# Kernel tuning notes

Hardware: AMD Instinct MI355X
Metric: run time of the kernel (lower is better)

Reference implementation:

```python
import math
import jax, jax.numpy as jnp
import numpy as np

B, N, M, C, H, POS = 2, 2048, 64, 256, 8, 6
D = C // H  # head_dim = 32
SCALE = 1.0 / math.sqrt(D)
LAMDA = 1.0


def setup_inputs() -> dict:
    key = jax.random.key(0)
    ks = jax.random.split(key, 15)
    s = 0.05
    return {
        "pairwise_g": jax.random.normal(ks[0], (B, N, N, POS), jnp.float32),
        "coset_functions": jax.random.normal(ks[1], (B, N, C), jnp.float32),
        "mask": jnp.ones((B, N), dtype=bool),
        "Wq": jax.random.normal(ks[2], (C, C), jnp.float32) * s,
        "bq": jax.random.normal(ks[3], (C,), jnp.float32) * s,
        "Wk": jax.random.normal(ks[4], (C, C), jnp.float32) * s,
        "bk": jax.random.normal(ks[5], (C,), jnp.float32) * s,
        "Wl": jax.random.normal(ks[6], (C, POS), jnp.float32) * s,
        "bl": jax.random.normal(ks[7], (C,), jnp.float32) * s,
        "u": jax.random.normal(ks[8], (H, D), jnp.float32) * s,
        "v": jax.random.normal(ks[9], (H, D), jnp.float32) * s,
        "Wi": jax.random.normal(ks[10], (C, C), jnp.float32) * s,
        "bi": jax.random.normal(ks[11], (C,), jnp.float32) * s,
        "Wo": jax.random.normal(ks[12], (C, C), jnp.float32) * s,
        "bo": jax.random.normal(ks[13], (C,), jnp.float32) * s,
    }


def reference(pairwise_g, coset_functions, mask, Wq, bq, Wk, bk, Wl, bl, u, v, Wi, bi, Wo, bo):
    # ---- extract_neighbourhoods (mc_samples=M, fill=1.0 -> k == k_ball, permutation irrelevant)
    dists = jnp.linalg.norm(pairwise_g, axis=-1)                      # (B,N,N)
    dists = jnp.where(mask[:, None, :], dists, jnp.float32(1e8))
    _, nbhd_idx = jax.lax.top_k(-dists, M)                            # (B,N,M) nearest neighbors
    nbhd_pg = jnp.take_along_axis(pairwise_g, nbhd_idx[..., None], axis=2)  # (B,N,M,POS)
    gather_rows = jax.vmap(lambda arr, ix: arr[ix])                   # gather along point axis per batch
    nbhd_cf = gather_rows(coset_functions, nbhd_idx)                  # (B,N,M,C)
    nbhd_mask = gather_rows(mask, nbhd_idx)                           # (B,N,M)

    # ---- RelativePositionKernel
    Q = (coset_functions @ Wq.T + bq).reshape(B, N, H, D).transpose(0, 2, 1, 3)  # (B,H,N,D)
    K = (coset_functions @ Wk.T + bk).reshape(B, N, H, D).transpose(0, 2, 1, 3)  # (B,H,N,D)
    e = (nbhd_pg @ Wl.T + bl).reshape(B, N, M, H, D)                  # (B,N,M,H,D)

    S = jnp.einsum('bhnd,bhkd->bhnk', Q, K)                           # dense scores (as original)
    Sg = jnp.take_along_axis(S, nbhd_idx[:, None, :, :], axis=3)      # (B,H,N,M)
    e_term = jnp.einsum('bnmhd,bhnd->bhnm', e, Q + v[None, :, None, :])
    uK = jnp.einsum('hd,bhkd->bhk', u, K)                             # (B,H,N)
    uKg = jnp.take_along_axis(uK[:, :, None, :], nbhd_idx[:, None, :, :], axis=3)  # (B,H,N,M)
    A = (Sg + LAMDA * e_term + uKg) * SCALE
    A = A.transpose(0, 2, 3, 1)                                       # (B,N,M,H)

    # ---- masked softmax over neighbors
    A = jnp.where(nbhd_mask[..., None], A, jnp.float32(-1e38))
    attn = jax.nn.softmax(A, axis=2)                                  # (B,N,M,H)

    # ---- value projection + weighted sum + output linear
    Vv = (nbhd_cf @ Wi.T + bi).reshape(B, N, M, H, D)                 # (B,N,M,H,D)
    out = jnp.einsum('bnmh,bnmhd->bnhd', attn, Vv).reshape(B, N, C)
    out = out @ Wo.T + bo                                             # (B,N,c_out)
    return out
```

## Files before the change

### kernel.cpp

```cpp
#include <hip/hip_runtime.h>
#include <stdint.h>

#define NB 2
#define NN 2048
#define MM 64
#define CC 256
#define HH 8
#define DD 32
#define PP 6
#define ATT_SCALE 0.17677669529663687f

typedef __attribute__((ext_vector_type(8))) short short8;
typedef __attribute__((ext_vector_type(4))) float f32x4;

__device__ __forceinline__ uint16_t f2bf(float f) {
  union { float f; uint32_t u; } c; c.f = f;
  return (uint16_t)((c.u + 0x7fffu + ((c.u >> 16) & 1u)) >> 16);
}
__device__ __forceinline__ float blo(uint32_t u) {
  union { uint32_t u; float f; } c; c.u = u << 16; return c.f;
}
__device__ __forceinline__ float bhi(uint32_t u) {
  union { uint32_t u; float f; } c; c.u = u & 0xffff0000u; return c.f;
}
__device__ __forceinline__ short8 pack8(float4 a, float4 b) {
  short8 r;
  r[0] = (short)f2bf(a.x); r[1] = (short)f2bf(a.y);
  r[2] = (short)f2bf(a.z); r[3] = (short)f2bf(a.w);
  r[4] = (short)f2bf(b.x); r[5] = (short)f2bf(b.y);
  r[6] = (short)f2bf(b.z); r[7] = (short)f2bf(b.w);
  return r;
}

__global__ __launch_bounds__(64) void k_gemm_qkv(
    const float* __restrict__ A,
    const float* __restrict__ W0, const float* __restrict__ W1, const float* __restrict__ W2,
    const float* __restrict__ b0, const float* __restrict__ b1, const float* __restrict__ b2,
    float* __restrict__ Qo, uint16_t* __restrict__ Ko, uint16_t* __restrict__ Vo) {
  const int z = blockIdx.z;
  const float* W = (z == 0) ? W0 : ((z == 1) ? W1 : W2);
  const float* bias = (z == 0) ? b0 : ((z == 1) ? b1 : b2);

  const int lane = threadIdx.x;
  const int m = lane & 15;
  const int quad = lane >> 4;
  const int row0 = blockIdx.x * 16;
  const int c0 = blockIdx.y * 64;

  f32x4 acc0 = {0.f, 0.f, 0.f, 0.f};
  f32x4 acc1 = {0.f, 0.f, 0.f, 0.f};
  f32x4 acc2 = {0.f, 0.f, 0.f, 0.f};
  f32x4 acc3 = {0.f, 0.f, 0.f, 0.f};

#pragma unroll
  for (int k0 = 0; k0 < CC; k0 += 32) {
    const float4* ap = (const float4*)(A + (size_t)(row0 + m) * CC + k0 + quad * 8);
    const float4* bp0 = (const float4*)(W + (size_t)(c0 + 0 + m) * CC + k0 + quad * 8);
    const float4* bp1 = (const float4*)(W + (size_t)(c0 + 16 + m) * CC + k0 + quad * 8);
    const float4* bp2 = (const float4*)(W + (size_t)(c0 + 32 + m) * CC + k0 + quad * 8);
    const float4* bp3 = (const float4*)(W + (size_t)(c0 + 48 + m) * CC + k0 + quad * 8);
    const short8 a = pack8(ap[0], ap[1]);
    const short8 f0 = pack8(bp0[0], bp0[1]);
    const short8 f1 = pack8(bp1[0], bp1[1]);
    const short8 f2 = pack8(bp2[0], bp2[1]);
    const short8 f3 = pack8(bp3[0], bp3[1]);
    acc0 = __builtin_amdgcn_mfma_f32_16x16x32_bf16(a, f0, acc0, 0, 0, 0);
    acc1 = __builtin_amdgcn_mfma_f32_16x16x32_bf16(a, f1, acc1, 0, 0, 0);
    acc2 = __builtin_amdgcn_mfma_f32_16x16x32_bf16(a, f2, acc2, 0, 0, 0);
    acc3 = __builtin_amdgcn_mfma_f32_16x16x32_bf16(a, f3, acc3, 0, 0, 0);
  }

  const int orow = row0 + quad * 4;
  f32x4 accs[4] = {acc0, acc1, acc2, acc3};
#pragma unroll
  for (int f = 0; f < 4; ++f) {
    const int col = c0 + f * 16 + m;
    const float bv = bias[col];
#pragma unroll
    for (int r = 0; r < 4; ++r) {
      const float val = accs[f][r] + bv;
      const size_t o = (size_t)(orow + r) * CC + col;
      if (z == 0) Qo[o] = val;
      else if (z == 1) Ko[o] = f2bf(val);
      else Vo[o] = f2bf(val);
    }
  }
}

__global__ __launch_bounds__(64) void k_gemm_out(const uint16_t* __restrict__ A,
                                                 const float* __restrict__ W,
                                                 const float* __restrict__ bias,
                                                 float* __restrict__ O) {
  const int lane = threadIdx.x;
  const int m = lane & 15;
  const int quad = lane >> 4;
  const int row0 = blockIdx.x * 16;
  const int c0 = blockIdx.y * 32;

  f32x4 acc0 = {0.f, 0.f, 0.f, 0.f};
  f32x4 acc1 = {0.f, 0.f, 0.f, 0.f};

#pragma unroll
  for (int k0 = 0; k0 < CC; k0 += 32) {
    const short8 a = *(const short8*)(A + (size_t)(row0 + m) * CC + k0 + quad * 8);
    const float4* bp0 = (const float4*)(W + (size_t)(c0 + 0 + m) * CC + k0 + quad * 8);
    const float4* bp1 = (const float4*)(W + (size_t)(c0 + 16 + m) * CC + k0 + quad * 8);
    const short8 f0 = pack8(bp0[0], bp0[1]);
    const short8 f1 = pack8(bp1[0], bp1[1]);
    acc0 = __builtin_amdgcn_mfma_f32_16x16x32_bf16(a, f0, acc0, 0, 0, 0);
    acc1 = __builtin_amdgcn_mfma_f32_16x16x32_bf16(a, f1, acc1, 0, 0, 0);
  }

  const int orow = row0 + quad * 4;
  f32x4 accs[2] = {acc0, acc1};
#pragma unroll
  for (int f = 0; f < 2; ++f) {
    const int col = c0 + f * 16 + m;
    const float bv = bias[col];
#pragma unroll
    for (int r = 0; r < 4; ++r) {
      O[(size_t)(orow + r) * CC + col] = accs[f][r] + bv;
    }
  }
}

__global__ __launch_bounds__(256) void k_fused(const float* __restrict__ pg,
                                               const float* __restrict__ Q,
                                               const uint16_t* __restrict__ K,
                                               const uint16_t* __restrict__ V,
                                               const float* __restrict__ Wl,
                                               const float* __restrict__ bl,
                                               const float* __restrict__ u,
                                               const float* __restrict__ v,
                                               uint16_t* __restrict__ attnV) {
  const int row = blockIdx.x;
  const int b = row >> 11;
  const int t = threadIdx.x;
  const int wave = t >> 6;
  const int lane = t & 63;

  __shared__ float s_mn[4], s_mx[4];
  __shared__ uint32_t s_wsum[4];
  __shared__ uint32_t s_hist[256];
  __shared__ uint32_t s_scan[256];
  __shared__ float s_cd[NN];
  __shared__ int   s_cj[NN];
  __shared__ int s_tbin;
  __shared__ uint32_t s_c0;
  __shared__ int s_cw;
  __shared__ int s_ct;
  __shared__ int s_idx[MM];
  __shared__ float s_npg[MM][7];
  __shared__ float s_qu[CC];
  __shared__ float s_wt[HH][8];
  __shared__ float s_sc[HH][MM];
  __shared__ float s_part[CC];

  const float qv_ = Q[(size_t)row * CC + t];
  s_qu[t] = qv_ + u[t];
  if (t < MM) s_idx[t] = t;

  const float4* base = (const float4*)(pg + (size_t)row * NN * PP);

  float d[8];
  float mn = 3.4e38f, mx = -3.4e38f;
#pragma unroll
  for (int i = 0; i < 4; i++) {
    const int j0 = i * 512 + 2 * t;
    const float4 qa = base[(size_t)(j0 >> 1) * 3 + 0];
    const float4 qb = base[(size_t)(j0 >> 1) * 3 + 1];
    const float4 qc = base[(size_t)(j0 >> 1) * 3 + 2];
    float s0 = __fmul_rn(qa.x, qa.x);
    s0 = __fadd_rn(s0, __fmul_rn(qa.y, qa.y));
    s0 = __fadd_rn(s0, __fmul_rn(qa.z, qa.z));
    s0 = __fadd_rn(s0, __fmul_rn(qa.w, qa.w));
    s0 = __fadd_rn(s0, __fmul_rn(qb.x, qb.x));
    s0 = __fadd_rn(s0, __fmul_rn(qb.y, qb.y));
    float s1 = __fmul_rn(qb.z, qb.z);
    s1 = __fadd_rn(s1, __fmul_rn(qb.w, qb.w));
    s1 = __fadd_rn(s1, __fmul_rn(qc.x, qc.x));
    s1 = __fadd_rn(s1, __fmul_rn(qc.y, qc.y));
    s1 = __fadd_rn(s1, __fmul_rn(qc.z, qc.z));
    s1 = __fadd_rn(s1, __fmul_rn(qc.w, qc.w));
    const float d0 = __fsqrt_rn(s0);
    const float d1 = __fsqrt_rn(s1);
    d[2 * i] = d0; d[2 * i + 1] = d1;
    mn = fminf(mn, fminf(d0, d1));
    mx = fmaxf(mx, fmaxf(d0, d1));
  }

#pragma unroll
  for (int off = 32; off; off >>= 1) {
    mn = fminf(mn, __shfl_xor(mn, off));
    mx = fmaxf(mx, __shfl_xor(mx, off));
  }
  if (lane == 0) { s_mn[wave] = mn; s_mx[wave] = mx; }
  s_hist[t] = 0;
  __syncthreads();
  mn = fminf(fminf(s_mn[0], s_mn[1]), fminf(s_mn[2], s_mn[3]));
  mx = fmaxf(fmaxf(s_mx[0], s_mx[1]), fmaxf(s_mx[2], s_mx[3]));
  const float range = mx - mn;
  const float scale = (range > 0.f) ? (256.0f / range) : 0.f;

  int bins[8];
#pragma unroll
  for (int i = 0; i < 8; i++) {
    int bn = (int)((d[i] - mn) * scale);
    bn = (bn > 255) ? 255 : (bn < 0 ? 0 : bn);
    bins[i] = bn;
    atomicAdd(&s_hist[bn], 1u);
  }
  __syncthreads();

  {
    uint32_t x = s_hist[t];
#pragma unroll
    for (int off = 1; off < 64; off <<= 1) {
      const uint32_t y = __shfl_up(x, off);
      if (lane >= off) x += y;
    }
    if (lane == 63) s_wsum[wave] = x;
    __syncthreads();
    uint32_t pre = 0;
    for (int w = 0; w < wave; w++) pre += s_wsum[w];
    x += pre;
    s_scan[t] = x;
  }
  if (t == 0) { s_cw = 0; s_ct = 0; }
  __syncthreads();

  if (s_scan[t] >= (uint32_t)MM && (t == 0 || s_scan[t - 1] < (uint32_t)MM)) {
    s_tbin = t;
    s_c0 = (t == 0) ? 0u : s_scan[t - 1];
  }
  __syncthreads();

  const int tbin = s_tbin;
  const int c0 = (int)s_c0;

#pragma unroll
  for (int i = 0; i < 8; i++) {
    const int j = (i >> 1) * 512 + 2 * t + (i & 1);
    if (bins[i] < tbin) {
      const int pos = atomicAdd(&s_cw, 1);
      if (pos < MM) s_idx[pos] = j;
    } else if (bins[i] == tbin) {
      const int pos = atomicAdd(&s_ct, 1);
      s_cd[pos] = d[i];
      s_cj[pos] = j;
    }
  }
  __syncthreads();

  if (t < 64) {
    const int cnt = s_ct;
    const int r = MM - c0;
    for (int it = 0; it < r; ++it) {
      float bd = 3.4e38f; int bj = 0x7fffffff; int bi = -1;
      for (int i = t; i < cnt; i += 64) {
        const float dd = s_cd[i]; const int jj = s_cj[i];
        if (dd < bd || (dd == bd && jj < bj)) { bd = dd; bj = jj; bi = i; }
      }
#pragma unroll
      for (int off = 32; off; off >>= 1) {
        const float od = __shfl_xor(bd, off);
        const int oj = __shfl_xor(bj, off);
        const int oi = __shfl_xor(bi, off);
        if (od < bd || (od == bd && oj < bj)) { bd = od; bj = oj; bi = oi; }
      }
      if (t == 0 && bi >= 0) {
        s_cd[bi] = 3.4e38f;
        s_idx[c0 + it] = bj;
      }
      __threadfence_block();
    }
  }
  __syncthreads();

  if (t < MM) {
    const int jj = s_idx[t] & (NN - 1);
    const float2* p = (const float2*)(pg + ((size_t)row * NN + (size_t)jj) * PP);
    const float2 p0 = p[0], p1 = p[1], p2 = p[2];
    s_npg[t][0] = p0.x; s_npg[t][1] = p0.y;
    s_npg[t][2] = p1.x; s_npg[t][3] = p1.y;
    s_npg[t][4] = p2.x; s_npg[t][5] = p2.y;
  }

  {
    const int h = t >> 5;
    const float qpv = qv_ + v[t];
    float part[7];
#pragma unroll
    for (int p = 0; p < 6; p++) part[p] = Wl[(size_t)t * PP + p] * qpv;
    part[6] = bl[t] * qpv;
#pragma unroll
    for (int off = 1; off < 32; off <<= 1) {
#pragma unroll
      for (int p = 0; p < 7; p++) part[p] += __shfl_xor(part[p], off);
    }
    if ((t & 31) == 0) {
#pragma unroll
      for (int p = 0; p < 7; p++) s_wt[h][p] = part[p];
    }
  }
  __syncthreads();

#pragma unroll
  for (int pr = 0; pr < 2; ++pr) {
    const int h = wave + pr * 4;
    const int m = lane;
    const int kidx = s_idx[m] & (NN - 1);
    const uint4* kr = (const uint4*)(K + ((size_t)(b * NN + kidx)) * CC + h * DD);
    float acc = s_wt[h][6];
#pragma unroll
    for (int p = 0; p < 6; p++) acc += s_npg[m][p] * s_wt[h][p];
    const float* qu = &s_qu[h * DD];
    float a2 = 0.f;
#pragma unroll
    for (int w4 = 0; w4 < 4; w4++) {
      const uint4 kv = kr[w4];
      const float* q8 = qu + w4 * 8;
      a2 += q8[0] * blo(kv.x) + q8[1] * bhi(kv.x)
          + q8[2] * blo(kv.y) + q8[3] * bhi(kv.y)
          + q8[4] * blo(kv.z) + q8[5] * bhi(kv.z)
          + q8[6] * blo(kv.w) + q8[7] * bhi(kv.w);
    }
    s_sc[h][m] = (acc + a2) * ATT_SCALE;
  }
  __syncthreads();

#pragma unroll
  for (int pr = 0; pr < 2; ++pr) {
    const int h = wave + pr * 4;
    const float x = s_sc[h][lane];
    float mxv = x;
#pragma unroll
    for (int off = 32; off; off >>= 1) mxv = fmaxf(mxv, __shfl_xor(mxv, off));
    const float e = expf(x - mxv);
    float sm = e;
#pragma unroll
    for (int off = 32; off; off >>= 1) sm += __shfl_xor(sm, off);
    s_sc[h][lane] = e / sm;
  }
  __syncthreads();

  {
    const int h2 = t >> 7;
    const int ci = (t & 127) * 2;
    const int h = ci >> 5;
    const uint32_t* Vb32 = (const uint32_t*)(V + (size_t)b * NN * CC);
    float a0 = 0.f, a1 = 0.f;
#pragma unroll 8
    for (int m = h2; m < MM; m += 2) {
      const uint32_t pv = Vb32[(size_t)(s_idx[m] & (NN - 1)) * (CC / 2) + (ci >> 1)];
      const float p = s_sc[h][m];
      a0 += p * blo(pv);
      a1 += p * bhi(pv);
    }
    if (h2 == 1) { s_part[ci] = a0; s_part[ci + 1] = a1; }
    __syncthreads();
    if (h2 == 0) {
      attnV[(size_t)row * CC + ci]     = f2bf(a0 + s_part[ci]);
      attnV[(size_t)row * CC + ci + 1] = f2bf(a1 + s_part[ci + 1]);
    }
  }
}

extern "C" void kernel_launch(void* const* d_in, const int* in_sizes, int n_in,
                              void* d_out, int out_size, void* d_ws, size_t ws_size,
                              hipStream_t stream) {
  const float* pg = (const float*)d_in[0];
  const float* cf = (const float*)d_in[1];
  const float* Wq = (const float*)d_in[3];
  const float* bq = (const float*)d_in[4];
  const float* Wk = (const float*)d_in[5];
  const float* bk = (const float*)d_in[6];
  const float* Wl = (const float*)d_in[7];
  const float* bl = (const float*)d_in[8];
  const float* u  = (const float*)d_in[9];
  const float* v  = (const float*)d_in[10];
  const float* Wi = (const float*)d_in[11];
  const float* bi = (const float*)d_in[12];
  const float* Wo = (const float*)d_in[13];
  const float* bo = (const float*)d_in[14];

  char* ws = (char*)d_ws;
  float* Q  = (float*)ws;
  uint16_t* K = (uint16_t*)(ws + (size_t)4 * (1 << 20));
  uint16_t* V = (uint16_t*)(ws + (size_t)6 * (1 << 20));
  uint16_t* aV = (uint16_t*)(ws + (size_t)8 * (1 << 20));
  float* out = (float*)d_out;

  hipLaunchKernelGGL(k_gemm_qkv, dim3(256, 4, 3), dim3(64), 0, stream,
                     cf, Wq, Wk, Wi, bq, bk, bi, Q, K, V);
  hipLaunchKernelGGL(k_fused, dim3(NB * NN), dim3(256), 0, stream,
                     pg, Q, K, V, Wl, bl, u, v, aV);
  hipLaunchKernelGGL(k_gemm_out, dim3(256, 8), dim3(64), 0, stream,
                     aV, Wo, bo, out);
}
```

Before: 359.0 us.

## Fuse output projection into fused kernel and refine top-k with second histogram pass

Folds the output linear layer into the per-row fused kernel: Wo is converted to bf16 in an extra z-slice of the QKV GEMM launch, and each thread then computes one output channel as a dot product over the attention result held in shared memory. This removes the separate output GEMM launch and the bf16 round-trip of the attention result. It also adds a second 256-bin histogram over the candidates in the threshold bin, so the serial wave-level argmin loop only has to resolve the few leftover elements. The trade-offs are extra synchronisation barriers per row and a per-row 128KB read of bf16 Wo from cache instead of MFMA-based batching.

```diff
diff --git a/kernel.cpp b/kernel.cpp
--- a/kernel.cpp
+++ b/kernel.cpp
@@ -35,13 +35,27 @@
 __global__ __launch_bounds__(64) void k_gemm_qkv(
     const float* __restrict__ A,
     const float* __restrict__ W0, const float* __restrict__ W1, const float* __restrict__ W2,
+    const float* __restrict__ Wo,
     const float* __restrict__ b0, const float* __restrict__ b1, const float* __restrict__ b2,
-    float* __restrict__ Qo, uint16_t* __restrict__ Ko, uint16_t* __restrict__ Vo) {
+    float* __restrict__ Qo, uint16_t* __restrict__ Ko, uint16_t* __restrict__ Vo,
+    uint16_t* __restrict__ wob) {
   const int z = blockIdx.z;
+  const int lane = threadIdx.x;
+
+  if (z == 3) {
+    if (blockIdx.y == 0) {
+      const int e = blockIdx.x * CC + lane * 4;
+      const float4 v4 = *(const float4*)(Wo + e);
+      ushort4 o;
+      o.x = f2bf(v4.x); o.y = f2bf(v4.y); o.z = f2bf(v4.z); o.w = f2bf(v4.w);
+      *(ushort4*)(wob + e) = o;
+    }
+    return;
+  }
+
   const float* W = (z == 0) ? W0 : ((z == 1) ? W1 : W2);
   const float* bias = (z == 0) ? b0 : ((z == 1) ? b1 : b2);
 
-  const int lane = threadIdx.x;
   const int m = lane & 15;
   const int quad = lane >> 4;
   const int row0 = blockIdx.x * 16;
@@ -87,43 +101,6 @@
   }
 }
 
-__global__ __launch_bounds__(64) void k_gemm_out(const uint16_t* __restrict__ A,
-                                                 const float* __restrict__ W,
-                                                 const float* __restrict__ bias,
-                                                 float* __restrict__ O) {
-  const int lane = threadIdx.x;
-  const int m = lane & 15;
-  const int quad = lane >> 4;
-  const int row0 = blockIdx.x * 16;
-  const int c0 = blockIdx.y * 32;
-
-  f32x4 acc0 = {0.f, 0.f, 0.f, 0.f};
-  f32x4 acc1 = {0.f, 0.f, 0.f, 0.f};
-
-#pragma unroll
-  for (int k0 = 0; k0 < CC; k0 += 32) {
-    const short8 a = *(const short8*)(A + (size_t)(row0 + m) * CC + k0 + quad * 8);
-    const float4* bp0 = (const float4*)(W + (size_t)(c0 + 0 + m) * CC + k0 + quad * 8);
-    const float4* bp1 = (const float4*)(W + (size_t)(c0 + 16 + m) * CC + k0 + quad * 8);
-    const short8 f0 = pack8(bp0[0], bp0[1]);
-    const short8 f1 = pack8(bp1[0], bp1[1]);
-    acc0 = __builtin_amdgcn_mfma_f32_16x16x32_bf16(a, f0, acc0, 0, 0, 0);
-    acc1 = __builtin_amdgcn_mfma_f32_16x16x32_bf16(a, f1, acc1, 0, 0, 0);
-  }
-
-  const int orow = row0 + quad * 4;
-  f32x4 accs[2] = {acc0, acc1};
-#pragma unroll
-  for (int f = 0; f < 2; ++f) {
-    const int col = c0 + f * 16 + m;
-    const float bv = bias[col];
-#pragma unroll
-    for (int r = 0; r < 4; ++r) {
-      O[(size_t)(orow + r) * CC + col] = accs[f][r] + bv;
-    }
-  }
-}
-
 __global__ __launch_bounds__(256) void k_fused(const float* __restrict__ pg,
                                                const float* __restrict__ Q,
                                                const uint16_t* __restrict__ K,
@@ -132,7 +109,9 @@
                                                const float* __restrict__ bl,
                                                const float* __restrict__ u,
                                                const float* __restrict__ v,
-                                               uint16_t* __restrict__ attnV) {
+                                               const uint16_t* __restrict__ wob,
+                                               const float* __restrict__ bo,
+                                               float* __restrict__ out) {
   const int row = blockIdx.x;
   const int b = row >> 11;
   const int t = threadIdx.x;
@@ -145,16 +124,16 @@
   __shared__ uint32_t s_scan[256];
   __shared__ float s_cd[NN];
   __shared__ int   s_cj[NN];
-  __shared__ int s_tbin;
-  __shared__ uint32_t s_c0;
-  __shared__ int s_cw;
-  __shared__ int s_ct;
+  __shared__ int s_tbin, s_tbin2;
+  __shared__ uint32_t s_c0, s_c02;
+  __shared__ int s_cw, s_ct, s_cw2;
   __shared__ int s_idx[MM];
   __shared__ float s_npg[MM][7];
   __shared__ float s_qu[CC];
   __shared__ float s_wt[HH][8];
   __shared__ float s_sc[HH][MM];
   __shared__ float s_part[CC];
+  __shared__ float s_av[CC];
 
   const float qv_ = Q[(size_t)row * CC + t];
   s_qu[t] = qv_ + u[t];
@@ -226,7 +205,7 @@
     x += pre;
     s_scan[t] = x;
   }
-  if (t == 0) { s_cw = 0; s_ct = 0; }
+  if (t == 0) { s_cw = 0; s_ct = 0; s_cw2 = 0; }
   __syncthreads();
 
   if (s_scan[t] >= (uint32_t)MM && (t == 0 || s_scan[t - 1] < (uint32_t)MM)) {
@@ -252,10 +231,64 @@
   }
   __syncthreads();
 
+  const int cnt = s_ct;
+  const int r = MM - c0;
+  const float binw = range * 0.00390625f;
+  const float lo = mn + (float)tbin * binw;
+  const float scale2 = (range > 0.f) ? (65536.0f / range) : 0.f;
+
+  s_hist[t] = 0;
+  __syncthreads();
+
+  for (int i = t; i < cnt; i += 256) {
+    int sb = (int)((s_cd[i] - lo) * scale2);
+    sb = (sb > 255) ? 255 : (sb < 0 ? 0 : sb);
+    atomicAdd(&s_hist[sb], 1u);
+  }
+  __syncthreads();
+
+  {
+    uint32_t x = s_hist[t];
+#pragma unroll
+    for (int off = 1; off < 64; off <<= 1) {
+      const uint32_t y = __shfl_up(x, off);
+      if (lane >= off) x += y;
+    }
+    if (lane == 63) s_wsum[wave] = x;
+    __syncthreads();
+    uint32_t pre = 0;
+    for (int w = 0; w < wave; w++) pre += s_wsum[w];
+    x += pre;
+    s_scan[t] = x;
+  }
+  __syncthreads();
+
+  if (s_scan[t] >= (uint32_t)r && (t == 0 || s_scan[t - 1] < (uint32_t)r)) {
+    s_tbin2 = t;
+    s_c02 = (t == 0) ? 0u : s_scan[t - 1];
+  }
+  __syncthreads();
+
+  const int tbin2 = s_tbin2;
+  const int sc0 = (int)s_c02;
+
+  for (int i = t; i < cnt; i += 256) {
+    const float dd = s_cd[i];
+    int sb = (int)((dd - lo) * scale2);
+    sb = (sb > 255) ? 255 : (sb < 0 ? 0 : sb);
+    if (sb < tbin2) {
+      const int pos = atomicAdd(&s_cw2, 1);
+      if (pos < r) s_idx[c0 + pos] = s_cj[i];
+      s_cd[i] = 3.4e38f;
+    } else if (sb > tbin2) {
+      s_cd[i] = 3.4e38f;
+    }
+  }
+  __syncthreads();
+
   if (t < 64) {
-    const int cnt = s_ct;
-    const int r = MM - c0;
-    for (int it = 0; it < r; ++it) {
+    const int r2 = r - sc0;
+    for (int it = 0; it < r2; ++it) {
       float bd = 3.4e38f; int bj = 0x7fffffff; int bi = -1;
       for (int i = t; i < cnt; i += 64) {
         const float dd = s_cd[i]; const int jj = s_cj[i];
@@ -270,7 +303,7 @@
       }
       if (t == 0 && bi >= 0) {
         s_cd[bi] = 3.4e38f;
-        s_idx[c0 + it] = bj;
+        s_idx[c0 + sc0 + it] = bj;
       }
       __threadfence_block();
     }
@@ -360,9 +393,27 @@
     if (h2 == 1) { s_part[ci] = a0; s_part[ci + 1] = a1; }
     __syncthreads();
     if (h2 == 0) {
-      attnV[(size_t)row * CC + ci]     = f2bf(a0 + s_part[ci]);
-      attnV[(size_t)row * CC + ci + 1] = f2bf(a1 + s_part[ci + 1]);
-    }
+      s_av[ci]     = a0 + s_part[ci];
+      s_av[ci + 1] = a1 + s_part[ci + 1];
+    }
+  }
+  __syncthreads();
+
+  {
+    const uint4* wrow = (const uint4*)(wob + (size_t)t * CC);
+    const float4* av4 = (const float4*)s_av;
+    float acc = 0.f;
+#pragma unroll 4
+    for (int k8 = 0; k8 < 32; k8++) {
+      const uint4 w8 = wrow[k8];
+      const float4 a0 = av4[k8 * 2];
+      const float4 a1 = av4[k8 * 2 + 1];
+      acc += a0.x * blo(w8.x) + a0.y * bhi(w8.x)
+           + a0.z * blo(w8.y) + a0.w * bhi(w8.y)
+           + a1.x * blo(w8.z) + a1.y * bhi(w8.z)
+           + a1.z * blo(w8.w) + a1.w * bhi(w8.w);
+    }
+    out[(size_t)row * CC + t] = acc + bo[t];
   }
 }
 
@@ -386,15 +437,13 @@
 
   char* ws = (char*)d_ws;
   float* Q  = (float*)ws;
-  uint16_t* K = (uint16_t*)(ws + (size_t)4 * (1 << 20));
-  uint16_t* V = (uint16_t*)(ws + (size_t)6 * (1 << 20));
-  uint16_t* aV = (uint16_t*)(ws + (size_t)8 * (1 << 20));
+  uint16_t* K   = (uint16_t*)(ws + (size_t)4 * (1 << 20));
+  uint16_t* V   = (uint16_t*)(ws + (size_t)6 * (1 << 20));
+  uint16_t* wob = (uint16_t*)(ws + (size_t)8 * (1 << 20));
   float* out = (float*)d_out;
 
-  hipLaunchKernelGGL(k_gemm_qkv, dim3(256, 4, 3), dim3(64), 0, stream,
-                     cf, Wq, Wk, Wi, bq, bk, bi, Q, K, V);
+  hipLaunchKernelGGL(k_gemm_qkv, dim3(256, 4, 4), dim3(64), 0, stream,
+                     cf, Wq, Wk, Wi, Wo, bq, bk, bi, Q, K, V, wob);
   hipLaunchKernelGGL(k_fused, dim3(NB * NN), dim3(256), 0, stream,
-                     pg, Q, K, V, Wl, bl, u, v, aV);
-  hipLaunchKernelGGL(k_gemm_out, dim3(256, 8), dim3(64), 0, stream,
-                     aV, Wo, bo, out);
-}
+                     pg, Q, K, V, Wl, bl, u, v, wob, bo, out);
+}
```

Result: slower. 394.6 us (+9.9%).

## Replace candidate buffer and serial argmin with multi-pass radix select for top-k

Applied to the files above, without the earlier changes.

Replaces the single-histogram threshold plus the serial 64-iteration wave argmin over the boundary bin with an iterative radix/histogram select. Passes refine on a scaled range, a finer sub-bin, then float bits and index bits, until the boundary digit resolves exactly. This removes the large shared candidate arrays (16KB), which may raise occupancy, and removes the serial tie-resolution loop. The cost is more block-wide syncs and histogram passes per row, and tie ordering depends on the passes.

```diff
diff --git a/kernel.cpp b/kernel.cpp
--- a/kernel.cpp
+++ b/kernel.cpp
@@ -124,6 +124,21 @@
   }
 }
 
+__device__ __forceinline__ int sel_digit(int pass, float dv, int jj,
+                                         float mn, float scl,
+                                         float lo2, float scl2) {
+  switch (pass) {
+    case 0: { int b = (int)((dv - mn) * scl);  return b < 0 ? 0 : (b > 255 ? 255 : b); }
+    case 1: { int b = (int)((dv - lo2) * scl2); return b < 0 ? 0 : (b > 255 ? 255 : b); }
+    case 2: return (int)((__float_as_uint(dv) >> 24) & 255u);
+    case 3: return (int)((__float_as_uint(dv) >> 16) & 255u);
+    case 4: return (int)((__float_as_uint(dv) >> 8) & 255u);
+    case 5: return (int)(__float_as_uint(dv) & 255u);
+    case 6: return jj >> 3;
+    default: return jj & 7;
+  }
+}
+
 __global__ __launch_bounds__(256) void k_fused(const float* __restrict__ pg,
                                                const float* __restrict__ Q,
                                                const uint16_t* __restrict__ K,
@@ -142,13 +157,9 @@
   __shared__ float s_mn[4], s_mx[4];
   __shared__ uint32_t s_wsum[4];
   __shared__ uint32_t s_hist[256];
-  __shared__ uint32_t s_scan[256];
-  __shared__ float s_cd[NN];
-  __shared__ int   s_cj[NN];
-  __shared__ int s_tbin;
-  __shared__ uint32_t s_c0;
+  __shared__ int s_tb, s_exact;
+  __shared__ uint32_t s_cb;
   __shared__ int s_cw;
-  __shared__ int s_ct;
   __shared__ int s_idx[MM];
   __shared__ float s_npg[MM][7];
   __shared__ float s_qu[CC];
@@ -195,25 +206,33 @@
     mx = fmaxf(mx, __shfl_xor(mx, off));
   }
   if (lane == 0) { s_mn[wave] = mn; s_mx[wave] = mx; }
-  s_hist[t] = 0;
+  if (t == 0) s_cw = 0;
   __syncthreads();
   mn = fminf(fminf(s_mn[0], s_mn[1]), fminf(s_mn[2], s_mn[3]));
   mx = fmaxf(fmaxf(s_mx[0], s_mx[1]), fmaxf(s_mx[2], s_mx[3]));
   const float range = mx - mn;
   const float scale = (range > 0.f) ? (256.0f / range) : 0.f;
 
-  int bins[8];
-#pragma unroll
-  for (int i = 0; i < 8; i++) {
-    int bn = (int)((d[i] - mn) * scale);
-    bn = (bn > 255) ? 255 : (bn < 0 ? 0 : bn);
-    bins[i] = bn;
-    atomicAdd(&s_hist[bn], 1u);
-  }
-  __syncthreads();
-
-  {
-    uint32_t x = s_hist[t];
+  uint32_t act = 0xFFu;
+  int need = MM;
+  float lo2 = 0.f, scl2 = 0.f;
+
+  for (int pass = 0; pass < 8; ++pass) {
+    s_hist[t] = 0;
+    if (t == 0) { s_tb = 255; s_exact = 0; s_cb = 0; }
+    __syncthreads();
+
+#pragma unroll
+    for (int i = 0; i < 8; i++) {
+      if (act & (1u << i)) {
+        const int jj = (i >> 1) * 512 + 2 * t + (i & 1);
+        atomicAdd(&s_hist[sel_digit(pass, d[i], jj, mn, scale, lo2, scl2)], 1u);
+      }
+    }
+    __syncthreads();
+
+    const uint32_t h = s_hist[t];
+    uint32_t x = h;
 #pragma unroll
     for (int off = 1; off < 64; off <<= 1) {
       const uint32_t y = __shfl_up(x, off);
@@ -224,56 +243,36 @@
     uint32_t pre = 0;
     for (int w = 0; w < wave; w++) pre += s_wsum[w];
     x += pre;
-    s_scan[t] = x;
-  }
-  if (t == 0) { s_cw = 0; s_ct = 0; }
-  __syncthreads();
-
-  if (s_scan[t] >= (uint32_t)MM && (t == 0 || s_scan[t - 1] < (uint32_t)MM)) {
-    s_tbin = t;
-    s_c0 = (t == 0) ? 0u : s_scan[t - 1];
-  }
-  __syncthreads();
-
-  const int tbin = s_tbin;
-  const int c0 = (int)s_c0;
-
-#pragma unroll
-  for (int i = 0; i < 8; i++) {
-    const int j = (i >> 1) * 512 + 2 * t + (i & 1);
-    if (bins[i] < tbin) {
-      const int pos = atomicAdd(&s_cw, 1);
-      if (pos < MM) s_idx[pos] = j;
-    } else if (bins[i] == tbin) {
-      const int pos = atomicAdd(&s_ct, 1);
-      s_cd[pos] = d[i];
-      s_cj[pos] = j;
-    }
-  }
-  __syncthreads();
-
-  if (t < 64) {
-    const int cnt = s_ct;
-    const int r = MM - c0;
-    for (int it = 0; it < r; ++it) {
-      float bd = 3.4e38f; int bj = 0x7fffffff; int bi = -1;
-      for (int i = t; i < cnt; i += 64) {
-        const float dd = s_cd[i]; const int jj = s_cj[i];
-        if (dd < bd || (dd == bd && jj < bj)) { bd = dd; bj = jj; bi = i; }
+    const uint32_t excl = x - h;
+    if ((int)excl < need && (int)x >= need) {
+      s_tb = t; s_cb = excl; s_exact = ((int)x == need) ? 1 : 0;
+    }
+    __syncthreads();
+
+    const int tb = s_tb;
+    const int exact = s_exact;
+
+#pragma unroll
+    for (int i = 0; i < 8; i++) {
+      if (act & (1u << i)) {
+        const int jj = (i >> 1) * 512 + 2 * t + (i & 1);
+        const int dg = sel_digit(pass, d[i], jj, mn, scale, lo2, scl2);
+        if (dg < tb || (dg == tb && exact)) {
+          const int pos = atomicAdd(&s_cw, 1);
+          if (pos < MM) s_idx[pos] = jj;
+          act &= ~(1u << i);
+        } else if (dg > tb) {
+          act &= ~(1u << i);
+        }
       }
-#pragma unroll
-      for (int off = 32; off; off >>= 1) {
-        const float od = __shfl_xor(bd, off);
-        const int oj = __shfl_xor(bj, off);
-        const int oi = __shfl_xor(bi, off);
-        if (od < bd || (od == bd && oj < bj)) { bd = od; bj = oj; bi = oi; }
-      }
-      if (t == 0 && bi >= 0) {
-        s_cd[bi] = 3.4e38f;
-        s_idx[c0 + it] = bj;
-      }
-      __threadfence_block();
-    }
+    }
+    need -= (int)s_cb;
+    if (exact) break;
+    if (pass == 0) {
+      lo2 = mn + (float)tb * (range * 0.00390625f);
+      scl2 = (range > 0.f) ? (65536.0f / range) : 0.f;
+    }
+    __syncthreads();
   }
   __syncthreads();
 
@@ -386,8 +385,8 @@
 
   char* ws = (char*)d_ws;
   float* Q  = (float*)ws;
-  uint16_t* K = (uint16_t*)(ws + (size_t)4 * (1 << 20));
-  uint16_t* V = (uint16_t*)(ws + (size_t)6 * (1 << 20));
+  uint16_t* K  = (uint16_t*)(ws + (size_t)4 * (1 << 20));
+  uint16_t* V  = (uint16_t*)(ws + (size_t)6 * (1 << 20));
   uint16_t* aV = (uint16_t*)(ws + (size_t)8 * (1 << 20));
   float* out = (float*)d_out;
 
```

Measured after the change: 361.2 us. About the same (+0.6%).
